# Kernel tuning notes

Measured on AMD Instinct MI355X. Metric: run time of the kernel, lower is better.

The kernel has to match this reference:

```python
import jax, jax.numpy as jnp
import numpy as np

FRAME_LENGTH = 800
FRAME_STEP = 200
FFT_LENGTH = 800


def _hann_window(n):
    # tf.signal.hann_window default: periodic=True -> 0.5 - 0.5*cos(2*pi*k/n)
    k = jnp.arange(n, dtype=jnp.float32)
    return 0.5 - 0.5 * jnp.cos(2.0 * np.pi * k / n)


def setup_inputs() -> dict:
    key = jax.random.key(0)
    signals = jax.random.normal(key, (16, 240000), dtype=jnp.float32)
    window = _hann_window(FRAME_LENGTH)  # fft_length == frame_length, no pad
    n = jnp.arange(FFT_LENGTH, dtype=jnp.float32)
    angles = -2.0 * np.pi * n[:, None] * n[None, :] / float(FFT_LENGTH)  # [k, n]
    dft_cos = jnp.cos(angles)
    dft_sin = jnp.sin(angles)
    return {"signals": signals, "window": window, "dft_cos": dft_cos, "dft_sin": dft_sin}


def reference(signals, window, dft_cos, dft_sin):
    # Frame the signal: [B, num_frames, frame_length] via gather (pad_end=False)
    signal_length = signals.shape[1]
    num_frames = (signal_length - FRAME_LENGTH) // FRAME_STEP + 1
    starts = jnp.arange(num_frames, dtype=jnp.int32) * FRAME_STEP
    offsets = jnp.arange(FRAME_LENGTH, dtype=jnp.int32)
    idx = starts[:, None] + offsets[None, :]          # [F, L]
    frames = signals[:, idx]                          # [B, F, L]
    windowed = frames * window[:FRAME_LENGTH]         # [B, F, L]
    # Dense real/imag DFT: out[b,f,k] = sum_n windowed[b,f,n] * dft[k,n]
    real = jnp.einsum('bfn,kn->bfk', windowed, dft_cos)
    imag = jnp.einsum('bfn,kn->bfk', windowed, dft_sin)
    bins = FFT_LENGTH // 2 + 1
    return jnp.stack([real[:, :, :bins], imag[:, :, :bins]], axis=-1)  # [B, F, bins, 2]
```

## Files before the change

kernel.cpp:

```cpp
#include <hip/hip_runtime.h>
#include <hip/hip_bf16.h>

#define NBATCH   16
#define SIGLEN   240000
#define FRAMES   1197
#define M_TOTAL  (NBATCH * FRAMES)
#define K_TOTAL  800
#define NBINS    401
#define NOUT     (2 * NBINS)
#define FSTEP    200

#define BM 128
#define BN 128
#define BK 32
#define NT (K_TOTAL / BK)
#define NTILES_N 7
#define NTILES_M 150
#define NWG      (NTILES_M * NTILES_N)
#define N_PAD    (NTILES_N * BN)

#define SIG_ELEMS ((size_t)NBATCH * SIGLEN)
#define B_WS_ELEMS ((size_t)N_PAD * K_TOTAL)
#define WS_NEEDED  ((SIG_ELEMS + B_WS_ELEMS) * 2)

#define TILE_B   8192
#define HALF_B   4096

typedef float  f32x4  __attribute__((ext_vector_type(4)));
typedef __bf16 bf16x8 __attribute__((ext_vector_type(8)));

static __device__ __forceinline__ unsigned f2bf_pair(float lo, float hi) {
    union { float f; unsigned u; } a, b;
    a.f = lo; b.f = hi;
    unsigned ua = (a.u + 0x7fffu + ((a.u >> 16) & 1u)) >> 16;
    unsigned ub = (b.u + 0x7fffu + ((b.u >> 16) & 1u)) >> 16;
    return ua | (ub << 16);
}

static __device__ __forceinline__ void gload_lds16(const void* g, void* l) {
    __builtin_amdgcn_global_load_lds(
        (const __attribute__((address_space(1))) void*)g,
        (__attribute__((address_space(3))) void*)l, 16, 0, 0);
}

__global__ __launch_bounds__(256) void prep_sig(
    const float* __restrict__ sig, ushort* __restrict__ sbf)
{
    size_t i8 = ((size_t)blockIdx.x * 256 + threadIdx.x) * 8;
    const float4 s0 = *(const float4*)(sig + i8);
    const float4 s1 = *(const float4*)(sig + i8 + 4);
    uint4 p;
    p.x = f2bf_pair(s0.x, s0.y);
    p.y = f2bf_pair(s0.z, s0.w);
    p.z = f2bf_pair(s1.x, s1.y);
    p.w = f2bf_pair(s1.z, s1.w);
    *(uint4*)(sbf + i8) = p;
}

__global__ __launch_bounds__(256) void prep_bw(
    const float* __restrict__ dcos, const float* __restrict__ dsin,
    const float* __restrict__ wnd, ushort* __restrict__ B)
{
    int idx = blockIdx.x * 256 + threadIdx.x;
    int j  = idx / 100;
    int c8 = (idx - j * 100) * 8;
    uint4 p;
    if (j < NOUT) {
        const float* src = ((j & 1) ? dsin : dcos) + (size_t)(j >> 1) * K_TOTAL + c8;
        const float4 s0 = *(const float4*)(src);
        const float4 s1 = *(const float4*)(src + 4);
        const float4 w0 = *(const float4*)(wnd + c8);
        const float4 w1 = *(const float4*)(wnd + c8 + 4);
        p.x = f2bf_pair(s0.x * w0.x, s0.y * w0.y);
        p.y = f2bf_pair(s0.z * w0.z, s0.w * w0.w);
        p.z = f2bf_pair(s1.x * w1.x, s1.y * w1.y);
        p.w = f2bf_pair(s1.z * w1.z, s1.w * w1.w);
    } else {
        p = make_uint4(0u, 0u, 0u, 0u);
    }
    *(uint4*)(B + (size_t)j * K_TOTAL + c8) = p;
}

__global__ __launch_bounds__(256) void stft_gemm_bf16(
    const ushort* __restrict__ sigbf, const ushort* __restrict__ B,
    float* __restrict__ out)
{
    __shared__ ushort As[2][BM * BK];
    __shared__ ushort Bs[2][BN * BK];

    const int tid = threadIdx.x;

    const int orig = blockIdx.x;
    const int xcd  = orig & 7;
    const int lid  = orig >> 3;
    const int bid  = (xcd < 2 ? xcd * 132 : 264 + (xcd - 2) * 131) + lid;

    const int mt = bid / NTILES_N;
    const int nt = bid - mt * NTILES_N;
    const int m0 = mt * BM;
    const int j0 = nt * BN;

    const int wave = tid >> 6;
    const int lane = tid & 63;
    const int wm   = wave >> 1;
    const int wn   = wave & 1;
    const int lr   = lane & 15;
    const int lg   = lane >> 4;

    const int sRow = tid >> 2;
    const int sCol = (tid & 3) * 8;

    int m1 = m0 + sRow;          if (m1 >= M_TOTAL) m1 = M_TOTAL - 1;
    int m2 = m0 + sRow + 64;     if (m2 >= M_TOTAL) m2 = M_TOTAL - 1;
    const int b1 = m1 / FRAMES, f1 = m1 - b1 * FRAMES;
    const int b2 = m2 / FRAMES, f2 = m2 - b2 * FRAMES;
    const ushort* aS0 = sigbf + (size_t)b1 * SIGLEN + f1 * FSTEP + sCol;
    const ushort* aS1 = sigbf + (size_t)b2 * SIGLEN + f2 * FSTEP + sCol;
    const ushort* bS0 = B + (size_t)(j0 + sRow) * K_TOTAL + sCol;
    const ushort* bS1 = bS0 + (size_t)64 * K_TOTAL;

    char* aD = (char*)&As[0][0] + wave * 1024;
    char* bD = (char*)&Bs[0][0] + wave * 1024;

#define STAGE(c, kofs) do {                                      \
        gload_lds16(aS0 + (kofs), aD + (c) * TILE_B);            \
        gload_lds16(aS1 + (kofs), aD + (c) * TILE_B + HALF_B);   \
        gload_lds16(bS0 + (kofs), bD + (c) * TILE_B);            \
        gload_lds16(bS1 + (kofs), bD + (c) * TILE_B + HALF_B);   \
    } while (0)

    f32x4 acc[4][4];
    #pragma unroll
    for (int i = 0; i < 4; ++i)
        #pragma unroll
        for (int jj = 0; jj < 4; ++jj)
            acc[i][jj] = (f32x4){0.f, 0.f, 0.f, 0.f};

    STAGE(0, 0);
    __syncthreads();

    int cur = 0;
    for (int t = 0; t < NT; ++t) {
        if (t + 1 < NT) STAGE(cur ^ 1, (t + 1) * BK);

        bf16x8 a[4], b[4];
        #pragma unroll
        for (int i = 0; i < 4; ++i)
            a[i] = *(const bf16x8*)&As[cur][(wm * 64 + i * 16 + lr) * BK + lg * 8];
        #pragma unroll
        for (int i = 0; i < 4; ++i)
            b[i] = *(const bf16x8*)&Bs[cur][(wn * 64 + i * 16 + lr) * BK + lg * 8];

        __builtin_amdgcn_s_setprio(1);
        #pragma unroll
        for (int i = 0; i < 4; ++i)
            #pragma unroll
            for (int jj = 0; jj < 4; ++jj)
                acc[i][jj] = __builtin_amdgcn_mfma_f32_16x16x32_bf16(a[i], b[jj], acc[i][jj], 0, 0, 0);
        __builtin_amdgcn_s_setprio(0);

        __syncthreads();
        cur ^= 1;
    }
#undef STAGE

    const int mb = m0 + wm * 64;
    const int jb = j0 + wn * 64;
    #pragma unroll
    for (int i = 0; i < 4; ++i) {
        #pragma unroll
        for (int jj = 0; jj < 4; ++jj) {
            int col = jb + jj * 16 + lr;
            if (col >= NOUT) continue;
            #pragma unroll
            for (int r = 0; r < 4; ++r) {
                int row = mb + i * 16 + lg * 4 + r;
                if (row < M_TOTAL)
                    out[(size_t)row * NOUT + col] = acc[i][jj][r];
            }
        }
    }
}

#define LDSS 40
__global__ __launch_bounds__(256) void stft_gemm_fb(
    const float* __restrict__ sig, const float* __restrict__ wnd,
    const float* __restrict__ dcos, const float* __restrict__ dsin,
    float* __restrict__ out)
{
    __shared__ ushort As[BM * LDSS];
    __shared__ ushort Bs[BN * LDSS];
    __shared__ int rowBase[BM];

    const int tid = threadIdx.x;
    const int bid = blockIdx.x;
    const int mt  = bid / NTILES_N;
    const int nt  = bid - mt * NTILES_N;
    const int m0  = mt * BM;
    const int j0  = nt * BN;

    if (tid < BM) {
        int m = m0 + tid;
        int v = -1;
        if (m < M_TOTAL) {
            int b  = m / FRAMES;
            int fl = m - b * FRAMES;
            v = b * SIGLEN + fl * FSTEP;
        }
        rowBase[tid] = v;
    }

    const int rS = tid >> 1;
    const int hS = tid & 1;

    const float* bRow = nullptr;
    {
        int j = j0 + rS;
        if (j < NOUT) {
            const float* srcm = (j & 1) ? dsin : dcos;
            bRow = srcm + (size_t)(j >> 1) * K_TOTAL;
        }
    }

    const int lane = tid & 63;
    const int wave = tid >> 6;
    const int wm   = wave >> 1;
    const int wn   = wave & 1;
    const int lr   = lane & 15;
    const int lg   = lane >> 4;

    f32x4 acc[4][4];
    #pragma unroll
    for (int i = 0; i < 4; ++i)
        #pragma unroll
        for (int jj = 0; jj < 4; ++jj)
            acc[i][jj] = (f32x4){0.f, 0.f, 0.f, 0.f};

    __syncthreads();

    for (int k0 = 0; k0 < K_TOTAL; k0 += BK) {
        {
            int base = rowBase[rS];
            float4 f0, f1, f2, f3;
            if (base >= 0) {
                const float4* sp = (const float4*)(sig + base + k0 + hS * 16);
                f0 = sp[0]; f1 = sp[1]; f2 = sp[2]; f3 = sp[3];
            } else {
                f0 = make_float4(0.f,0.f,0.f,0.f); f1 = f0; f2 = f0; f3 = f0;
            }
            const float4* wp = (const float4*)(wnd + k0 + hS * 16);
            float4 w0 = wp[0], w1 = wp[1], w2 = wp[2], w3 = wp[3];
            uint4 p0, p1;
            p0.x = f2bf_pair(f0.x * w0.x, f0.y * w0.y);
            p0.y = f2bf_pair(f0.z * w0.z, f0.w * w0.w);
            p0.z = f2bf_pair(f1.x * w1.x, f1.y * w1.y);
            p0.w = f2bf_pair(f1.z * w1.z, f1.w * w1.w);
            p1.x = f2bf_pair(f2.x * w2.x, f2.y * w2.y);
            p1.y = f2bf_pair(f2.z * w2.z, f2.w * w2.w);
            p1.z = f2bf_pair(f3.x * w3.x, f3.y * w3.y);
            p1.w = f2bf_pair(f3.z * w3.z, f3.w * w3.w);
            uint4* dst = (uint4*)&As[rS * LDSS + hS * 16];
            dst[0] = p0; dst[1] = p1;
        }
        {
            uint4 p0, p1;
            if (bRow) {
                const float4* sp = (const float4*)(bRow + k0 + hS * 16);
                float4 f0 = sp[0], f1 = sp[1], f2 = sp[2], f3 = sp[3];
                p0.x = f2bf_pair(f0.x, f0.y);
                p0.y = f2bf_pair(f0.z, f0.w);
                p0.z = f2bf_pair(f1.x, f1.y);
                p0.w = f2bf_pair(f1.z, f1.w);
                p1.x = f2bf_pair(f2.x, f2.y);
                p1.y = f2bf_pair(f2.z, f2.w);
                p1.z = f2bf_pair(f3.x, f3.y);
                p1.w = f2bf_pair(f3.z, f3.w);
            } else {
                p0 = make_uint4(0u,0u,0u,0u); p1 = p0;
            }
            uint4* dst = (uint4*)&Bs[rS * LDSS + hS * 16];
            dst[0] = p0; dst[1] = p1;
        }
        __syncthreads();

        bf16x8 a[4], b[4];
        #pragma unroll
        for (int i = 0; i < 4; ++i)
            a[i] = *(const bf16x8*)&As[(wm * 64 + i * 16 + lr) * LDSS + lg * 8];
        #pragma unroll
        for (int i = 0; i < 4; ++i)
            b[i] = *(const bf16x8*)&Bs[(wn * 64 + i * 16 + lr) * LDSS + lg * 8];
        #pragma unroll
        for (int i = 0; i < 4; ++i)
            #pragma unroll
            for (int jj = 0; jj < 4; ++jj)
                acc[i][jj] = __builtin_amdgcn_mfma_f32_16x16x32_bf16(a[i], b[jj], acc[i][jj], 0, 0, 0);

        __syncthreads();
    }

    const int mb = m0 + wm * 64;
    const int jb = j0 + wn * 64;
    #pragma unroll
    for (int i = 0; i < 4; ++i) {
        #pragma unroll
        for (int jj = 0; jj < 4; ++jj) {
            int col = jb + jj * 16 + lr;
            if (col >= NOUT) continue;
            #pragma unroll
            for (int r = 0; r < 4; ++r) {
                int row = mb + i * 16 + lg * 4 + r;
                if (row < M_TOTAL)
                    out[(size_t)row * NOUT + col] = acc[i][jj][r];
            }
        }
    }
}

extern "C" void kernel_launch(void* const* d_in, const int* in_sizes, int n_in,
                              void* d_out, int out_size, void* d_ws, size_t ws_size,
                              hipStream_t stream) {
    const float* sig  = (const float*)d_in[0];
    const float* wnd  = (const float*)d_in[1];
    const float* dcos = (const float*)d_in[2];
    const float* dsin = (const float*)d_in[3];
    float* out = (float*)d_out;

    if (ws_size >= WS_NEEDED && d_ws != nullptr) {
        ushort* sbf = (ushort*)d_ws;
        ushort* Bws = sbf + SIG_ELEMS;
        prep_sig<<<dim3(SIG_ELEMS / 8 / 256), dim3(256), 0, stream>>>(sig, sbf);
        prep_bw<<<dim3(N_PAD * 100 / 256), dim3(256), 0, stream>>>(dcos, dsin, wnd, Bws);
        stft_gemm_bf16<<<dim3(NWG), dim3(256), 0, stream>>>(sbf, Bws, out);
    } else {
        stft_gemm_fb<<<dim3(NWG), dim3(256), 0, stream>>>(sig, wnd, dcos, dsin, out);
    }
}
```

Measured before the change: 66.18 us.

## Load GEMM fragments directly from global into registers and merge prep kernels

```diff
diff --git a/kernel.cpp b/kernel.cpp
--- a/kernel.cpp
+++ b/kernel.cpp
@@ -23,8 +23,8 @@
 #define B_WS_ELEMS ((size_t)N_PAD * K_TOTAL)
 #define WS_NEEDED  ((SIG_ELEMS + B_WS_ELEMS) * 2)
 
-#define TILE_B   8192
-#define HALF_B   4096
+#define PREP_SIG_BLOCKS 1875
+#define PREP_B_BLOCKS   350
 
 typedef float  f32x4  __attribute__((ext_vector_type(4)));
 typedef __bf16 bf16x8 __attribute__((ext_vector_type(8)));
@@ -37,57 +37,48 @@
     return ua | (ub << 16);
 }
 
-static __device__ __forceinline__ void gload_lds16(const void* g, void* l) {
-    __builtin_amdgcn_global_load_lds(
-        (const __attribute__((address_space(1))) void*)g,
-        (__attribute__((address_space(3))) void*)l, 16, 0, 0);
-}
-
-__global__ __launch_bounds__(256) void prep_sig(
-    const float* __restrict__ sig, ushort* __restrict__ sbf)
+__global__ __launch_bounds__(256) void prep_all(
+    const float* __restrict__ sig, const float* __restrict__ wnd,
+    const float* __restrict__ dcos, const float* __restrict__ dsin,
+    ushort* __restrict__ sbf, ushort* __restrict__ B)
 {
-    size_t i8 = ((size_t)blockIdx.x * 256 + threadIdx.x) * 8;
-    const float4 s0 = *(const float4*)(sig + i8);
-    const float4 s1 = *(const float4*)(sig + i8 + 4);
-    uint4 p;
-    p.x = f2bf_pair(s0.x, s0.y);
-    p.y = f2bf_pair(s0.z, s0.w);
-    p.z = f2bf_pair(s1.x, s1.y);
-    p.w = f2bf_pair(s1.z, s1.w);
-    *(uint4*)(sbf + i8) = p;
-}
-
-__global__ __launch_bounds__(256) void prep_bw(
-    const float* __restrict__ dcos, const float* __restrict__ dsin,
-    const float* __restrict__ wnd, ushort* __restrict__ B)
-{
-    int idx = blockIdx.x * 256 + threadIdx.x;
-    int j  = idx / 100;
-    int c8 = (idx - j * 100) * 8;
-    uint4 p;
-    if (j < NOUT) {
-        const float* src = ((j & 1) ? dsin : dcos) + (size_t)(j >> 1) * K_TOTAL + c8;
-        const float4 s0 = *(const float4*)(src);
-        const float4 s1 = *(const float4*)(src + 4);
-        const float4 w0 = *(const float4*)(wnd + c8);
-        const float4 w1 = *(const float4*)(wnd + c8 + 4);
-        p.x = f2bf_pair(s0.x * w0.x, s0.y * w0.y);
-        p.y = f2bf_pair(s0.z * w0.z, s0.w * w0.w);
-        p.z = f2bf_pair(s1.x * w1.x, s1.y * w1.y);
-        p.w = f2bf_pair(s1.z * w1.z, s1.w * w1.w);
+    const int blk = blockIdx.x;
+    if (blk < PREP_SIG_BLOCKS) {
+        size_t i8 = ((size_t)blk * 256 + threadIdx.x) * 8;
+        const float4 s0 = *(const float4*)(sig + i8);
+        const float4 s1 = *(const float4*)(sig + i8 + 4);
+        uint4 p;
+        p.x = f2bf_pair(s0.x, s0.y);
+        p.y = f2bf_pair(s0.z, s0.w);
+        p.z = f2bf_pair(s1.x, s1.y);
+        p.w = f2bf_pair(s1.z, s1.w);
+        *(uint4*)(sbf + i8) = p;
     } else {
-        p = make_uint4(0u, 0u, 0u, 0u);
-    }
-    *(uint4*)(B + (size_t)j * K_TOTAL + c8) = p;
-}
-
-__global__ __launch_bounds__(256) void stft_gemm_bf16(
-    const ushort* __restrict__ sigbf, const ushort* __restrict__ B,
+        int idx = (blk - PREP_SIG_BLOCKS) * 256 + threadIdx.x;
+        int j  = idx / 100;
+        int c8 = (idx - j * 100) * 8;
+        uint4 p;
+        if (j < NOUT) {
+            const float* src = ((j & 1) ? dsin : dcos) + (size_t)(j >> 1) * K_TOTAL + c8;
+            const float4 s0 = *(const float4*)(src);
+            const float4 s1 = *(const float4*)(src + 4);
+            const float4 w0 = *(const float4*)(wnd + c8);
+            const float4 w1 = *(const float4*)(wnd + c8 + 4);
+            p.x = f2bf_pair(s0.x * w0.x, s0.y * w0.y);
+            p.y = f2bf_pair(s0.z * w0.z, s0.w * w0.w);
+            p.z = f2bf_pair(s1.x * w1.x, s1.y * w1.y);
+            p.w = f2bf_pair(s1.z * w1.z, s1.w * w1.w);
+        } else {
+            p = make_uint4(0u, 0u, 0u, 0u);
+        }
+        *(uint4*)(B + (size_t)j * K_TOTAL + c8) = p;
+    }
+}
+
+__global__ __launch_bounds__(256) void stft_gemm_reg(
+    const ushort* __restrict__ sigbf, const ushort* __restrict__ Bw,
     float* __restrict__ out)
 {
-    __shared__ ushort As[2][BM * BK];
-    __shared__ ushort Bs[2][BN * BK];
-
     const int tid = threadIdx.x;
 
     const int orig = blockIdx.x;
@@ -107,27 +98,16 @@
     const int lr   = lane & 15;
     const int lg   = lane >> 4;
 
-    const int sRow = tid >> 2;
-    const int sCol = (tid & 3) * 8;
-
-    int m1 = m0 + sRow;          if (m1 >= M_TOTAL) m1 = M_TOTAL - 1;
-    int m2 = m0 + sRow + 64;     if (m2 >= M_TOTAL) m2 = M_TOTAL - 1;
-    const int b1 = m1 / FRAMES, f1 = m1 - b1 * FRAMES;
-    const int b2 = m2 / FRAMES, f2 = m2 - b2 * FRAMES;
-    const ushort* aS0 = sigbf + (size_t)b1 * SIGLEN + f1 * FSTEP + sCol;
-    const ushort* aS1 = sigbf + (size_t)b2 * SIGLEN + f2 * FSTEP + sCol;
-    const ushort* bS0 = B + (size_t)(j0 + sRow) * K_TOTAL + sCol;
-    const ushort* bS1 = bS0 + (size_t)64 * K_TOTAL;
-
-    char* aD = (char*)&As[0][0] + wave * 1024;
-    char* bD = (char*)&Bs[0][0] + wave * 1024;
-
-#define STAGE(c, kofs) do {                                      \
-        gload_lds16(aS0 + (kofs), aD + (c) * TILE_B);            \
-        gload_lds16(aS1 + (kofs), aD + (c) * TILE_B + HALF_B);   \
-        gload_lds16(bS0 + (kofs), bD + (c) * TILE_B);            \
-        gload_lds16(bS1 + (kofs), bD + (c) * TILE_B + HALF_B);   \
-    } while (0)
+    const ushort* aP[4];
+    const ushort* bP[4];
+    #pragma unroll
+    for (int i = 0; i < 4; ++i) {
+        int row = m0 + wm * 64 + i * 16 + lr;
+        if (row >= M_TOTAL) row = M_TOTAL - 1;
+        int bb = row / FRAMES, ff = row - bb * FRAMES;
+        aP[i] = sigbf + (size_t)bb * SIGLEN + ff * FSTEP + lg * 8;
+        bP[i] = Bw + (size_t)(j0 + wn * 64 + i * 16 + lr) * K_TOTAL + lg * 8;
+    }
 
     f32x4 acc[4][4];
     #pragma unroll
@@ -136,33 +116,39 @@
         for (int jj = 0; jj < 4; ++jj)
             acc[i][jj] = (f32x4){0.f, 0.f, 0.f, 0.f};
 
-    STAGE(0, 0);
-    __syncthreads();
-
-    int cur = 0;
-    for (int t = 0; t < NT; ++t) {
-        if (t + 1 < NT) STAGE(cur ^ 1, (t + 1) * BK);
-
-        bf16x8 a[4], b[4];
-        #pragma unroll
-        for (int i = 0; i < 4; ++i)
-            a[i] = *(const bf16x8*)&As[cur][(wm * 64 + i * 16 + lr) * BK + lg * 8];
-        #pragma unroll
-        for (int i = 0; i < 4; ++i)
-            b[i] = *(const bf16x8*)&Bs[cur][(wn * 64 + i * 16 + lr) * BK + lg * 8];
-
-        __builtin_amdgcn_s_setprio(1);
-        #pragma unroll
-        for (int i = 0; i < 4; ++i)
-            #pragma unroll
-            for (int jj = 0; jj < 4; ++jj)
-                acc[i][jj] = __builtin_amdgcn_mfma_f32_16x16x32_bf16(a[i], b[jj], acc[i][jj], 0, 0, 0);
-        __builtin_amdgcn_s_setprio(0);
-
-        __syncthreads();
-        cur ^= 1;
-    }
-#undef STAGE
+#define LOADF(A_, B_, kofs) do {                                   \
+        _Pragma("unroll")                                          \
+        for (int i = 0; i < 4; ++i) {                              \
+            A_[i] = *(const bf16x8*)(aP[i] + (kofs));              \
+            B_[i] = *(const bf16x8*)(bP[i] + (kofs));              \
+        }                                                          \
+    } while (0)
+
+#define MM(A_, B_) do {                                            \
+        __builtin_amdgcn_s_setprio(1);                             \
+        _Pragma("unroll")                                          \
+        for (int i = 0; i < 4; ++i)                                \
+            _Pragma("unroll")                                      \
+            for (int jj = 0; jj < 4; ++jj)                         \
+                acc[i][jj] = __builtin_amdgcn_mfma_f32_16x16x32_bf16( \
+                    A_[i], B_[jj], acc[i][jj], 0, 0, 0);           \
+        __builtin_amdgcn_s_setprio(0);                             \
+    } while (0)
+
+    bf16x8 aX[4], bX[4], aY[4], bY[4];
+    LOADF(aX, bX, 0);
+
+    #pragma unroll 1
+    for (int t = 0; t < NT - 1; t += 2) {
+        LOADF(aY, bY, (t + 1) * BK);
+        MM(aX, bX);
+        LOADF(aX, bX, (t + 2) * BK);
+        MM(aY, bY);
+    }
+    MM(aX, bX);
+
+#undef LOADF
+#undef MM
 
     const int mb = m0 + wm * 64;
     const int jb = j0 + wn * 64;
@@ -329,9 +315,9 @@
     if (ws_size >= WS_NEEDED && d_ws != nullptr) {
         ushort* sbf = (ushort*)d_ws;
         ushort* Bws = sbf + SIG_ELEMS;
-        prep_sig<<<dim3(SIG_ELEMS / 8 / 256), dim3(256), 0, stream>>>(sig, sbf);
-        prep_bw<<<dim3(N_PAD * 100 / 256), dim3(256), 0, stream>>>(dcos, dsin, wnd, Bws);
-        stft_gemm_bf16<<<dim3(NWG), dim3(256), 0, stream>>>(sbf, Bws, out);
+        prep_all<<<dim3(PREP_SIG_BLOCKS + PREP_B_BLOCKS), dim3(256), 0, stream>>>(
+            sig, wnd, dcos, dsin, sbf, Bws);
+        stft_gemm_reg<<<dim3(NWG), dim3(256), 0, stream>>>(sbf, Bws, out);
     } else {
         stft_gemm_fb<<<dim3(NWG), dim3(256), 0, stream>>>(sig, wnd, dcos, dsin, out);
     }
```

Measured after the change: 85.97 us. 29.9% more time.
